# Kernel optimization log

Hardware: AMD Instinct MI355X
Metric: run time of the kernel (lower is better)

Reference implementation:

```python
import jax, jax.numpy as jnp
import numpy as np

DIM = 512
B, S = 4, 2048


def _linear_params(key, d_in, d_out):
    kw, kb = jax.random.split(key)
    bound = 1.0 / np.sqrt(d_in)
    W = jax.random.uniform(kw, (d_out, d_in), minval=-bound, maxval=bound, dtype=jnp.float32)
    b = jax.random.uniform(kb, (d_out,), minval=-bound, maxval=bound, dtype=jnp.float32)
    return W, b


def setup_inputs() -> dict:
    key = jax.random.key(0)
    ks = jax.random.split(key, 6)
    x = jax.random.normal(ks[0], (B, S, DIM), dtype=jnp.float32)
    Wq, bq = _linear_params(ks[1], DIM, DIM)
    Wk, bk = _linear_params(ks[2], DIM, DIM)
    Wv, bv = _linear_params(ks[3], DIM, DIM)
    W1, b1 = _linear_params(ks[4], DIM, 4 * DIM)
    W2, b2 = _linear_params(ks[5], 4 * DIM, DIM)
    return {"x": x, "Wq": Wq, "bq": bq, "Wk": Wk, "bk": bk,
            "Wv": Wv, "bv": bv, "W1": W1, "b1": b1, "W2": W2, "b2": b2}


def reference(x, Wq, bq, Wk, bk, Wv, bv, W1, b1, W2, b2):
    # q, k, v projections (torch Linear: x @ W.T + b)
    q = x @ Wq.T + bq          # [B, S, D]
    k = x @ Wk.T + bk
    v = x @ Wv.T + bv
    # unscaled attention, exactly as in the source (no 1/sqrt(d))
    scores = jnp.einsum('bsd,btd->bst', q, k)   # [B, S, S]
    attn = jax.nn.softmax(scores, axis=-1) @ v  # [B, S, D]
    # 2-layer FFN with ReLU
    h = jax.nn.relu(attn @ W1.T + b1)           # [B, S, 4D]
    return h @ W2.T + b2                        # [B, S, D]
```

## Files before the change

kernel.cpp:

```cpp
#include <hip/hip_runtime.h>
#include <hip/hip_bf16.h>

typedef _Float16  f16x8  __attribute__((ext_vector_type(8)));
typedef float     f32x4  __attribute__((ext_vector_type(4)));
typedef unsigned short u16;
typedef u16       u16x4  __attribute__((ext_vector_type(4)));
typedef u16       u16x8  __attribute__((ext_vector_type(8)));

__device__ __forceinline__ u16 f2h_bits(float f) {
    union { _Float16 h; u16 u; } v; v.h = (_Float16)f; return v.u;
}

__global__ __launch_bounds__(256)
void cvt_all(const float* __restrict__ x,
             const float* __restrict__ Wq, const float* __restrict__ Wk,
             const float* __restrict__ Wv, const float* __restrict__ W1,
             const float* __restrict__ W2, const float* __restrict__ bq,
             const float* __restrict__ bk, const float* __restrict__ bv,
             u16* __restrict__ x16, u16* __restrict__ Wqkv16,
             u16* __restrict__ W116, u16* __restrict__ W216, float* __restrict__ bqkv) {
    const int i = blockIdx.x * 256 + threadIdx.x;
    constexpr int X4 = 8192 * 512 / 4;
    constexpr int S = 512 * 512 / 4, L = 2048 * 512 / 4;
    const float* src; u16* dst; int j;
    if      (i < X4)                 { src = x;  dst = x16;            j = i;                  }
    else if (i < X4 + S)             { src = Wq; dst = Wqkv16;         j = i - X4;             }
    else if (i < X4 + 2 * S)         { src = Wk; dst = Wqkv16 + 4 * S; j = i - X4 - S;         }
    else if (i < X4 + 3 * S)         { src = Wv; dst = Wqkv16 + 8 * S; j = i - X4 - 2 * S;     }
    else if (i < X4 + 3 * S + L)     { src = W1; dst = W116;           j = i - X4 - 3 * S;     }
    else if (i < X4 + 3 * S + 2 * L) { src = W2; dst = W216;           j = i - X4 - 3 * S - L; }
    else if (i < X4 + 3 * S + 2 * L + 384) {
        const int g = (i - X4 - 3 * S - 2 * L) * 4;
#pragma unroll
        for (int t = 0; t < 4; ++t) {
            const int e = g + t;
            bqkv[e] = (e < 512) ? bq[e] : (e < 1024 ? bk[e - 512] : bv[e - 1024]);
        }
        return;
    } else return;
    f32x4 v = ((const f32x4*)src)[j];
    u16x4 h;
#pragma unroll
    for (int t = 0; t < 4; ++t) h[t] = f2h_bits(v[t]);
    ((u16x4*)dst)[j] = h;
}

template<int ROWS>
__device__ __forceinline__ void stage_rows(const u16* __restrict__ g0, int ld, u16* lds, int wl) {
    const int l = threadIdx.x & 63;
    constexpr int CH = ROWS / 64;
#pragma unroll
    for (int i = 0; i < CH; ++i) {
        const int base = (wl * CH + i) << 10;
        const int off  = base + (l << 4);
        const int row  = off >> 6;
        const int cb   = off & 63;
        const u16* g = g0 + (size_t)row * ld + (cb >> 1);
        __builtin_amdgcn_global_load_lds((const __attribute__((address_space(1))) void*)g,
                                         (__attribute__((address_space(3))) void*)((char*)lds + base),
                                         16, 0, 0);
    }
}

template<int BN, int SPLITK, bool RELU, int OMODE, bool PVS, typename TC>
__global__ __launch_bounds__(256 * SPLITK, 4)
void gemm16(const u16* __restrict__ Ag, const u16* __restrict__ Bg,
            const float* __restrict__ bias, TC* __restrict__ C,
            void* __restrict__ xtra, const void* __restrict__ xtra2,
            int K, int lda, int ldb, int ldc,
            long sA, long sB, long sC)
{
    const int nx = gridDim.x, ny = gridDim.y;
    const int nwg = nx * ny * gridDim.z;
    int bid = blockIdx.x + nx * (blockIdx.y + ny * blockIdx.z);
    int swz = (bid & 7) * (nwg >> 3) + (bid >> 3);
    const int n0 = (swz % nx) * BN; swz /= nx;
    const int m0 = (swz % ny) * 128;
    const int bz = swz / ny;

    constexpr int FR = (BN == 128) ? 4 : 2;
    constexpr int ATILE = 128 * 32;
    constexpr int BTILE = BN * 32;
    constexpr int BUFSZ = ATILE + BTILE;
    __shared__ __align__(16) u16 smem[SPLITK * 2 * BUFSZ];

    const int l  = threadIdx.x & 63, w = threadIdx.x >> 6;
    const int kw = (SPLITK == 2) ? (w >> 2) : 0;
    const int wl = w & 3;
    const int wr = (BN == 128) ? (wl >> 1) * 64 : wl * 32;
    const int wc = (BN == 128) ? (wl & 1) * 64 : 0;
    const int lr = l & 15, kg = l >> 4;

    const int Kh = K / SPLITK;
    const int kb = kw * Kh;

    const u16* Ab = Ag + (size_t)bz * sA + (size_t)m0 * lda + kb;
    const u16* Bb = Bg + (size_t)bz * sB + (size_t)n0 * ldb + kb;
    const float* Cb = PVS ? ((const float*)xtra2 + (size_t)bz * 2048 * 32) : nullptr;
    C += (size_t)bz * sC;

    u16* mybuf = smem + kw * 2 * BUFSZ;

    auto stage = [&](int buf, int k0) {
        u16* s = mybuf + buf * BUFSZ;
        stage_rows<128>(Ab + k0, lda, s, wl);
        stage_rows<BN>(Bb + k0, ldb, s + ATILE, wl);
    };

    f32x4 acc[FR][4] = {};
    f32x4 tmp[FR][4] = {};
    auto compute = [&](int buf) {
        const u16* sA = mybuf + buf * BUFSZ;
        const u16* sB = sA + ATILE;
        f16x8 a[FR], b[4];
#pragma unroll
        for (int i = 0; i < FR; ++i) a[i] = *(const f16x8*)&sA[(wr + i * 16 + lr) * 32 + kg * 8];
#pragma unroll
        for (int i = 0; i < 4; ++i)  b[i] = *(const f16x8*)&sB[(wc + i * 16 + lr) * 32 + kg * 8];
#pragma unroll
        for (int mi = 0; mi < FR; ++mi)
#pragma unroll
            for (int ni = 0; ni < 4; ++ni) {
                if constexpr (PVS)
                    tmp[mi][ni] = __builtin_amdgcn_mfma_f32_16x16x32_f16(a[mi], b[ni], tmp[mi][ni], 0, 0, 0);
                else
                    acc[mi][ni] = __builtin_amdgcn_mfma_f32_16x16x32_f16(a[mi], b[ni], acc[mi][ni], 0, 0, 0);
            }
    };

    stage(0, 0);
    __syncthreads();
    int cur = 0;
    for (int k0 = 0; k0 < Kh; k0 += 32) {
        if (k0 + 32 < Kh) stage(cur ^ 1, k0 + 32);
        compute(cur);
        if constexpr (PVS) {
            if (k0 & 32) {
                const int cb = (kb + k0) >> 6;
#pragma unroll
                for (int mi = 0; mi < FR; ++mi) {
                    const int mrow = m0 + wr + mi * 16 + kg * 4;
                    f32x4 cf4;
#pragma unroll
                    for (int j = 0; j < 4; ++j) cf4[j] = Cb[(size_t)(mrow + j) * 32 + cb];
#pragma unroll
                    for (int ni = 0; ni < 4; ++ni) {
#pragma unroll
                        for (int j = 0; j < 4; ++j) acc[mi][ni][j] += cf4[j] * tmp[mi][ni][j];
                        tmp[mi][ni] = f32x4{0.f, 0.f, 0.f, 0.f};
                    }
                }
            }
        }
        __syncthreads();
        cur ^= 1;
    }

    if constexpr (SPLITK == 2) {
        float* red = (float*)smem;
        const int slot = (wl * 64 + l) * (FR * 4);
        if (kw == 1) {
#pragma unroll
            for (int mi = 0; mi < FR; ++mi)
#pragma unroll
                for (int ni = 0; ni < 4; ++ni)
                    *(f32x4*)&red[(slot + mi * 4 + ni) * 4] = acc[mi][ni];
        }
        __syncthreads();
        if (kw == 1) return;
#pragma unroll
        for (int mi = 0; mi < FR; ++mi)
#pragma unroll
            for (int ni = 0; ni < 4; ++ni)
                acc[mi][ni] += *(const f32x4*)&red[(slot + mi * 4 + ni) * 4];
    }

    if constexpr (OMODE == 5) {
        float* MB = (float*)xtra + (size_t)bz * 2048 * 32;
        float* SB = (float*)const_cast<void*>(xtra2);
        SB += (size_t)bz * 2048 * 32;
        const int cb = (n0 + wc) >> 6;
#pragma unroll
        for (int mi = 0; mi < FR; ++mi) {
            const int mbase = m0 + wr + mi * 16 + kg * 4;
#pragma unroll
            for (int j = 0; j < 4; ++j) {
                float rmax = fmaxf(fmaxf(acc[mi][0][j], acc[mi][1][j]),
                                   fmaxf(acc[mi][2][j], acc[mi][3][j]));
                rmax = fmaxf(rmax, __shfl_xor(rmax, 1));
                rmax = fmaxf(rmax, __shfl_xor(rmax, 2));
                rmax = fmaxf(rmax, __shfl_xor(rmax, 4));
                rmax = fmaxf(rmax, __shfl_xor(rmax, 8));
                float p[4]; float lsum = 0.0f;
#pragma unroll
                for (int ni = 0; ni < 4; ++ni) { p[ni] = __expf(acc[mi][ni][j] - rmax); lsum += p[ni]; }
                lsum += __shfl_xor(lsum, 1);
                lsum += __shfl_xor(lsum, 2);
                lsum += __shfl_xor(lsum, 4);
                lsum += __shfl_xor(lsum, 8);
                const int row = mbase + j;
                if (lr == 0) {
                    MB[(size_t)row * 32 + cb] = rmax;
                    SB[(size_t)row * 32 + cb] = lsum;
                }
#pragma unroll
                for (int ni = 0; ni < 4; ++ni)
                    ((u16*)C)[(size_t)row * ldc + (n0 + wc + ni * 16 + lr)] = f2h_bits(p[ni]);
            }
        }
        return;
    }

#pragma unroll
    for (int mi = 0; mi < FR; ++mi) {
        const int mbase = m0 + wr + mi * 16 + kg * 4;
#pragma unroll
        for (int ni = 0; ni < 4; ++ni) {
            const int n = n0 + wc + ni * 16 + lr;
            const float bv = bias ? bias[n] : 0.0f;
            if constexpr (OMODE == 4) {
                if (n0 < 1024) {
#pragma unroll
                    for (int j = 0; j < 4; ++j)
                        ((u16*)C)[(size_t)(mbase + j) * ldc + n] = f2h_bits(acc[mi][ni][j] + bv);
                } else {
                    const int d  = n - 1024;
                    const int bb = mbase >> 11;
                    const int s  = mbase & 2047;
                    u16x4 o;
#pragma unroll
                    for (int j = 0; j < 4; ++j) o[j] = f2h_bits(acc[mi][ni][j] + bv);
                    *(u16x4*)((u16*)xtra + ((size_t)bb * 512 + d) * 2048 + s) = o;
                }
            } else {
#pragma unroll
                for (int j = 0; j < 4; ++j) {
                    float x = acc[mi][ni][j] + bv;
                    if constexpr (RELU) x = fmaxf(x, 0.0f);
                    const size_t idx = (size_t)(mbase + j) * ldc + n;
                    if constexpr (OMODE == 0) C[idx] = x;
                    else                      ((u16*)C)[idx] = f2h_bits(x);
                }
            }
        }
    }
}

__global__ __launch_bounds__(256)
void softmax_stats(const float* __restrict__ MB, const float* __restrict__ SB,
                   float* __restrict__ Cf) {
    const int row = blockIdx.x * 256 + threadIdx.x;
    const f32x4* mbp = (const f32x4*)(MB + (size_t)row * 32);
    const f32x4* sbp = (const f32x4*)(SB + (size_t)row * 32);
    f32x4 mv[8], sv[8];
#pragma unroll
    for (int i = 0; i < 8; ++i) { mv[i] = mbp[i]; sv[i] = sbp[i]; }
    float m = mv[0][0];
#pragma unroll
    for (int i = 0; i < 8; ++i)
#pragma unroll
        for (int j = 0; j < 4; ++j) m = fmaxf(m, mv[i][j]);
    float e[8][4]; float s = 0.0f;
#pragma unroll
    for (int i = 0; i < 8; ++i)
#pragma unroll
        for (int j = 0; j < 4; ++j) { e[i][j] = __expf(mv[i][j] - m); s += sv[i][j] * e[i][j]; }
    const float inv = 1.0f / s;
    f32x4* cp = (f32x4*)(Cf + (size_t)row * 32);
#pragma unroll
    for (int i = 0; i < 8; ++i) {
        f32x4 o;
#pragma unroll
        for (int j = 0; j < 4; ++j) o[j] = e[i][j] * inv;
        cp[i] = o;
    }
}

extern "C" void kernel_launch(void* const* d_in, const int* in_sizes, int n_in,
                              void* d_out, int out_size, void* d_ws, size_t ws_size,
                              hipStream_t stream) {
    const float* x  = (const float*)d_in[0];
    const float* Wq = (const float*)d_in[1];
    const float* bq = (const float*)d_in[2];
    const float* Wk = (const float*)d_in[3];
    const float* bk = (const float*)d_in[4];
    const float* Wv = (const float*)d_in[5];
    const float* bv = (const float*)d_in[6];
    const float* W1 = (const float*)d_in[7];
    const float* b1 = (const float*)d_in[8];
    const float* W2 = (const float*)d_in[9];
    const float* b2 = (const float*)d_in[10];
    float* out = (float*)d_out;

    char* ws = (char*)d_ws;
    size_t off = 0;
    auto alloc = [&](size_t bytes) { void* p = ws + off; off += (bytes + 255) & ~(size_t)255; return p; };
    u16* x16    = (u16*)alloc(8192ull * 512 * 2);
    u16* Wqkv16 = (u16*)alloc(1536ull * 512 * 2);
    u16* W116   = (u16*)alloc(2048ull * 512 * 2);
    u16* W216   = (u16*)alloc(512ull * 2048 * 2);
    float* bqkv = (float*)alloc(1536 * 4);
    u16* qk     = (u16*)alloc(8192ull * 1024 * 2);
    u16* p16    = (u16*)alloc(4ull * 2048 * 2048 * 2);
    u16* vt     = (u16*)alloc(4ull * 512 * 2048 * 2);
    float* mb   = (float*)alloc(8192ull * 32 * 4);
    float* sb   = (float*)alloc(8192ull * 32 * 4);
    float* cf   = (float*)alloc(8192ull * 32 * 4);
    u16* attn = x16;
    u16* h    = p16;
    if (ws_size < off) return;

    dim3 blk(256), blk2(512);

    cvt_all<<<dim3(6914), blk, 0, stream>>>(x, Wq, Wk, Wv, W1, W2, bq, bk, bv,
                                            x16, Wqkv16, W116, W216, bqkv);

    gemm16<128, 1, false, 4, false, u16><<<dim3(12, 64, 1), blk, 0, stream>>>(
        x16, Wqkv16, bqkv, qk, vt, nullptr, 512, 512, 512, 1024, 0, 0, 0);
    gemm16<128, 1, false, 5, false, u16><<<dim3(16, 16, 4), blk, 0, stream>>>(
        qk, qk + 512, nullptr, p16, mb, sb, 512, 1024, 1024, 2048,
        2048L * 1024, 2048L * 1024, 2048L * 2048);
    softmax_stats<<<dim3(32), blk, 0, stream>>>(mb, sb, cf);
    gemm16<64, 2, false, 2, true, u16><<<dim3(8, 16, 4), blk2, 0, stream>>>(
        p16, vt, nullptr, attn, nullptr, cf, 2048, 2048, 2048, 512,
        2048L * 2048, 512L * 2048, 2048L * 512);
    gemm16<128, 1, true, 2, false, u16><<<dim3(16, 64, 1), blk, 0, stream>>>(
        attn, W116, b1, h, nullptr, nullptr, 512, 512, 512, 2048, 0, 0, 0);
    gemm16<64, 2, false, 0, false, float><<<dim3(8, 64, 1), blk2, 0, stream>>>(
        h, W216, b2, out, nullptr, nullptr, 2048, 2048, 2048, 512, 0, 0, 0);
}
```

Before: 183.1 us.

## Add BM template, use 64x64 tiles for PV and FFN2 GEMMs, transpose softmax coefficients

Adds a BM template parameter so the GEMM can use 64-row tiles with 2 waves per K-split. The PV and second FFN GEMMs switch from 128x64 tiles in 512-thread blocks to 64x64 tiles in 256-thread blocks, which doubles the grid size to fill more CUs. The softmax per-chunk coefficients are now stored transposed (chunk-major). This lets the PV kernel load them as one vector per fragment, prefetched before compute, instead of four scalar strided loads. Smaller tiles reduce data reuse per block and raise global/L2 traffic.

```diff
diff --git a/kernel.cpp b/kernel.cpp
--- a/kernel.cpp
+++ b/kernel.cpp
@@ -45,10 +45,10 @@
     ((u16x4*)dst)[j] = h;
 }
 
-template<int ROWS>
+template<int ROWS, int NW>
 __device__ __forceinline__ void stage_rows(const u16* __restrict__ g0, int ld, u16* lds, int wl) {
     const int l = threadIdx.x & 63;
-    constexpr int CH = ROWS / 64;
+    constexpr int CH = ROWS / 16 / NW;
 #pragma unroll
     for (int i = 0; i < CH; ++i) {
         const int base = (wl * CH + i) << 10;
@@ -62,8 +62,8 @@
     }
 }
 
-template<int BN, int SPLITK, bool RELU, int OMODE, bool PVS, typename TC>
-__global__ __launch_bounds__(256 * SPLITK, 4)
+template<int BM, int BN, int SPLITK, bool RELU, int OMODE, bool PVS, typename TC>
+__global__ __launch_bounds__((BM == 64 ? 128 : 256) * SPLITK, 4)
 void gemm16(const u16* __restrict__ Ag, const u16* __restrict__ Bg,
             const float* __restrict__ bias, TC* __restrict__ C,
             void* __restrict__ xtra, const void* __restrict__ xtra2,
@@ -75,18 +75,19 @@
     int bid = blockIdx.x + nx * (blockIdx.y + ny * blockIdx.z);
     int swz = (bid & 7) * (nwg >> 3) + (bid >> 3);
     const int n0 = (swz % nx) * BN; swz /= nx;
-    const int m0 = (swz % ny) * 128;
+    const int m0 = (swz % ny) * BM;
     const int bz = swz / ny;
 
+    constexpr int WPK = (BM == 64) ? 2 : 4;
     constexpr int FR = (BN == 128) ? 4 : 2;
-    constexpr int ATILE = 128 * 32;
+    constexpr int ATILE = BM * 32;
     constexpr int BTILE = BN * 32;
     constexpr int BUFSZ = ATILE + BTILE;
     __shared__ __align__(16) u16 smem[SPLITK * 2 * BUFSZ];
 
     const int l  = threadIdx.x & 63, w = threadIdx.x >> 6;
-    const int kw = (SPLITK == 2) ? (w >> 2) : 0;
-    const int wl = w & 3;
+    const int kw = (SPLITK == 2) ? (w / WPK) : 0;
+    const int wl = w % WPK;
     const int wr = (BN == 128) ? (wl >> 1) * 64 : wl * 32;
     const int wc = (BN == 128) ? (wl & 1) * 64 : 0;
     const int lr = l & 15, kg = l >> 4;
@@ -96,19 +97,20 @@
 
     const u16* Ab = Ag + (size_t)bz * sA + (size_t)m0 * lda + kb;
     const u16* Bb = Bg + (size_t)bz * sB + (size_t)n0 * ldb + kb;
-    const float* Cb = PVS ? ((const float*)xtra2 + (size_t)bz * 2048 * 32) : nullptr;
+    const float* Cb = PVS ? ((const float*)xtra2 + (size_t)bz * 32 * 2048) : nullptr;
     C += (size_t)bz * sC;
 
     u16* mybuf = smem + kw * 2 * BUFSZ;
 
     auto stage = [&](int buf, int k0) {
         u16* s = mybuf + buf * BUFSZ;
-        stage_rows<128>(Ab + k0, lda, s, wl);
-        stage_rows<BN>(Bb + k0, ldb, s + ATILE, wl);
+        stage_rows<BM, WPK>(Ab + k0, lda, s, wl);
+        stage_rows<BN, WPK>(Bb + k0, ldb, s + ATILE, wl);
     };
 
     f32x4 acc[FR][4] = {};
     f32x4 tmp[FR][4] = {};
+    f32x4 cfp[FR];
     auto compute = [&](int buf) {
         const u16* sA = mybuf + buf * BUFSZ;
         const u16* sB = sA + ATILE;
@@ -133,23 +135,25 @@
     int cur = 0;
     for (int k0 = 0; k0 < Kh; k0 += 32) {
         if (k0 + 32 < Kh) stage(cur ^ 1, k0 + 32);
+        if constexpr (PVS) {
+            if ((k0 & 32) == 0) {
+                const int cb = (kb + k0) >> 6;
+#pragma unroll
+                for (int mi = 0; mi < FR; ++mi)
+                    cfp[mi] = *(const f32x4*)&Cb[(size_t)cb * 2048 + (m0 + wr + mi * 16 + kg * 4)];
+            }
+        }
         compute(cur);
         if constexpr (PVS) {
             if (k0 & 32) {
-                const int cb = (kb + k0) >> 6;
-#pragma unroll
-                for (int mi = 0; mi < FR; ++mi) {
-                    const int mrow = m0 + wr + mi * 16 + kg * 4;
-                    f32x4 cf4;
-#pragma unroll
-                    for (int j = 0; j < 4; ++j) cf4[j] = Cb[(size_t)(mrow + j) * 32 + cb];
+#pragma unroll
+                for (int mi = 0; mi < FR; ++mi)
 #pragma unroll
                     for (int ni = 0; ni < 4; ++ni) {
 #pragma unroll
-                        for (int j = 0; j < 4; ++j) acc[mi][ni][j] += cf4[j] * tmp[mi][ni][j];
+                        for (int j = 0; j < 4; ++j) acc[mi][ni][j] += cfp[mi][j] * tmp[mi][ni][j];
                         tmp[mi][ni] = f32x4{0.f, 0.f, 0.f, 0.f};
                     }
-                }
             }
         }
         __syncthreads();
@@ -266,14 +270,12 @@
 #pragma unroll
         for (int j = 0; j < 4; ++j) { e[i][j] = __expf(mv[i][j] - m); s += sv[i][j] * e[i][j]; }
     const float inv = 1.0f / s;
-    f32x4* cp = (f32x4*)(Cf + (size_t)row * 32);
-#pragma unroll
-    for (int i = 0; i < 8; ++i) {
-        f32x4 o;
-#pragma unroll
-        for (int j = 0; j < 4; ++j) o[j] = e[i][j] * inv;
-        cp[i] = o;
-    }
+    const int bz = row >> 11, sr = row & 2047;
+    float* cp = Cf + (size_t)bz * 32 * 2048 + sr;
+#pragma unroll
+    for (int i = 0; i < 8; ++i)
+#pragma unroll
+        for (int j = 0; j < 4; ++j) cp[(size_t)(i * 4 + j) * 2048] = e[i][j] * inv;
 }
 
 extern "C" void kernel_launch(void* const* d_in, const int* in_sizes, int n_in,
@@ -315,17 +317,17 @@
     cvt_all<<<dim3(6914), blk, 0, stream>>>(x, Wq, Wk, Wv, W1, W2, bq, bk, bv,
                                             x16, Wqkv16, W116, W216, bqkv);
 
-    gemm16<128, 1, false, 4, false, u16><<<dim3(12, 64, 1), blk, 0, stream>>>(
+    gemm16<128, 128, 1, false, 4, false, u16><<<dim3(12, 64, 1), blk, 0, stream>>>(
         x16, Wqkv16, bqkv, qk, vt, nullptr, 512, 512, 512, 1024, 0, 0, 0);
-    gemm16<128, 1, false, 5, false, u16><<<dim3(16, 16, 4), blk, 0, stream>>>(
+    gemm16<128, 128, 1, false, 5, false, u16><<<dim3(16, 16, 4), blk, 0, stream>>>(
         qk, qk + 512, nullptr, p16, mb, sb, 512, 1024, 1024, 2048,
         2048L * 1024, 2048L * 1024, 2048L * 2048);
     softmax_stats<<<dim3(32), blk, 0, stream>>>(mb, sb, cf);
-    gemm16<64, 2, false, 2, true, u16><<<dim3(8, 16, 4), blk2, 0, stream>>>(
+    gemm16<64, 64, 2, false, 2, true, u16><<<dim3(8, 32, 4), blk, 0, stream>>>(
         p16, vt, nullptr, attn, nullptr, cf, 2048, 2048, 2048, 512,
         2048L * 2048, 512L * 2048, 2048L * 512);
-    gemm16<128, 1, true, 2, false, u16><<<dim3(16, 64, 1), blk, 0, stream>>>(
+    gemm16<128, 128, 1, true, 2, false, u16><<<dim3(16, 64, 1), blk, 0, stream>>>(
         attn, W116, b1, h, nullptr, nullptr, 512, 512, 512, 2048, 0, 0, 0);
-    gemm16<64, 2, false, 0, false, float><<<dim3(8, 64, 1), blk2, 0, stream>>>(
+    gemm16<64, 64, 2, false, 0, false, float><<<dim3(8, 128, 1), blk, 0, stream>>>(
         h, W216, b2, out, nullptr, nullptr, 2048, 2048, 2048, 512, 0, 0, 0);
 }
```

Result: slower. 188.9 us (+3.2%).
